# Optimization experiments

Measured on AMD Instinct MI355X. Metric: run time of the kernel, lower is better.

## Reference

```python
import jax, jax.numpy as jnp
import numpy as np

B = 4096      # number of graphs (segments)
D = 256       # node feature dim
N = B * 64    # total nodes across the batch


def setup_inputs() -> dict:
    key = jax.random.key(0)
    x = jax.random.normal(key, (N, D), dtype=jnp.float32)
    # ragged per-graph node counts: strictly positive, sum exactly to N
    rng = np.random.default_rng(0)
    sizes = 1 + rng.multinomial(N - B, np.full(B, 1.0 / B))
    feature_size_list = jnp.asarray(sizes, dtype=jnp.int64)
    return {"x": x, "feature_size_list": feature_size_list}


def reference(x, feature_size_list):
    # Fused segment-mean: one pass over x instead of a Python loop with cat.
    num_segments = feature_size_list.shape[0]  # static
    seg_ids = jnp.repeat(
        jnp.arange(num_segments), feature_size_list, total_repeat_length=x.shape[0]
    )
    sums = jax.ops.segment_sum(x, seg_ids, num_segments=num_segments)  # [B, D]
    return sums / feature_size_list[:, None].astype(x.dtype)
```

## Files before the change

kernel.cpp:

```cpp
#include <hip/hip_runtime.h>


#define NSEG 4096

__global__ __launch_bounds__(256) void scan_offsets_kernel(
    const int* __restrict__ sizes, int* __restrict__ offsets) {
    const int CHUNK = NSEG / 256;
    int tid = threadIdx.x;
    int base = tid * CHUNK;

    int local[CHUNK];
    int sum = 0;
#pragma unroll
    for (int i = 0; i < CHUNK; ++i) local[i] = sizes[base + i];
#pragma unroll
    for (int i = 0; i < CHUNK; ++i) {
        int v = local[i];
        local[i] = sum;
        sum += v;
    }

    __shared__ int sh[256];
    sh[tid] = sum;
    __syncthreads();
    for (int off = 1; off < 256; off <<= 1) {
        int v = (tid >= off) ? sh[tid - off] : 0;
        __syncthreads();
        sh[tid] += v;
        __syncthreads();
    }
    int excl = (tid == 0) ? 0 : sh[tid - 1];
#pragma unroll
    for (int i = 0; i < CHUNK; ++i) offsets[base + i] = excl + local[i];
}

__global__ __launch_bounds__(256) void seg_mean_kernel(
    const float* __restrict__ x,
    const int* __restrict__ sizes,
    const int* __restrict__ offsets,
    float* __restrict__ out) {
    int b = blockIdx.x;
    int size = sizes[b];
    size_t start = (size_t)offsets[b];

    int tx = threadIdx.x & 63;
    int ty = threadIdx.x >> 6;

    const float4* xr = reinterpret_cast<const float4*>(x) + start * 64 + tx;

    float4 a0 = make_float4(0.f, 0.f, 0.f, 0.f);
    float4 a1 = make_float4(0.f, 0.f, 0.f, 0.f);

    int r = ty;
    for (; r + 8 <= size; r += 8) {
        float4 v0 = xr[(size_t)r * 64];
        float4 v1 = xr[(size_t)(r + 4) * 64];
        a0.x += v0.x; a0.y += v0.y; a0.z += v0.z; a0.w += v0.w;
        a1.x += v1.x; a1.y += v1.y; a1.z += v1.z; a1.w += v1.w;
    }
    for (; r < size; r += 4) {
        float4 v0 = xr[(size_t)r * 64];
        a0.x += v0.x; a0.y += v0.y; a0.z += v0.z; a0.w += v0.w;
    }
    a0.x += a1.x; a0.y += a1.y; a0.z += a1.z; a0.w += a1.w;

    __shared__ float4 sh[256];
    sh[threadIdx.x] = a0;
    __syncthreads();

    if (ty == 0) {
        float4 b0 = sh[tx];
        float4 b1 = sh[tx + 64];
        float4 b2 = sh[tx + 128];
        float4 b3 = sh[tx + 192];
        float fs = (float)size;
        float4 o;
        o.x = (b0.x + b1.x + b2.x + b3.x) / fs;
        o.y = (b0.y + b1.y + b2.y + b3.y) / fs;
        o.z = (b0.z + b1.z + b2.z + b3.z) / fs;
        o.w = (b0.w + b1.w + b2.w + b3.w) / fs;
        reinterpret_cast<float4*>(out)[(size_t)b * 64 + tx] = o;
    }
}

extern "C" void kernel_launch(void* const* d_in, const int* in_sizes, int n_in,
                              void* d_out, int out_size, void* d_ws, size_t ws_size,
                              hipStream_t stream) {
    const float* x = (const float*)d_in[0];
    const int* sizes = (const int*)d_in[1];
    float* out = (float*)d_out;
    int* offsets = (int*)d_ws;

    scan_offsets_kernel<<<1, 256, 0, stream>>>(sizes, offsets);
    seg_mean_kernel<<<NSEG, 256, 0, stream>>>(x, sizes, offsets, out);
}
```

Measured before the change: 50.90 us.

## Fuse offset scan into segment-mean kernel and deepen load unrolling

Removes the separate single-block scan kernel. Each block now computes its own start offset by summing all preceding segment sizes with a wave-shuffle reduction, which saves a launch and a serial dependency. The cost is redundant work that grows with the block index, up to about 4096 int reads for the last block. The row loop is also unrolled to four independent accumulators, and loads and stores use nontemporal hints.

```diff
diff --git a/kernel.cpp b/kernel.cpp
--- a/kernel.cpp
+++ b/kernel.cpp
@@ -3,83 +3,68 @@
 
 #define NSEG 4096
 
-__global__ __launch_bounds__(256) void scan_offsets_kernel(
-    const int* __restrict__ sizes, int* __restrict__ offsets) {
-    const int CHUNK = NSEG / 256;
-    int tid = threadIdx.x;
-    int base = tid * CHUNK;
+typedef float f32x4 __attribute__((ext_vector_type(4)));
 
-    int local[CHUNK];
-    int sum = 0;
-#pragma unroll
-    for (int i = 0; i < CHUNK; ++i) local[i] = sizes[base + i];
-#pragma unroll
-    for (int i = 0; i < CHUNK; ++i) {
-        int v = local[i];
-        local[i] = sum;
-        sum += v;
-    }
-
-    __shared__ int sh[256];
-    sh[tid] = sum;
-    __syncthreads();
-    for (int off = 1; off < 256; off <<= 1) {
-        int v = (tid >= off) ? sh[tid - off] : 0;
-        __syncthreads();
-        sh[tid] += v;
-        __syncthreads();
-    }
-    int excl = (tid == 0) ? 0 : sh[tid - 1];
-#pragma unroll
-    for (int i = 0; i < CHUNK; ++i) offsets[base + i] = excl + local[i];
-}
-
-__global__ __launch_bounds__(256) void seg_mean_kernel(
+__global__ __launch_bounds__(256) void seg_mean_fused_kernel(
     const float* __restrict__ x,
     const int* __restrict__ sizes,
-    const int* __restrict__ offsets,
     float* __restrict__ out) {
-    int b = blockIdx.x;
-    int size = sizes[b];
-    size_t start = (size_t)offsets[b];
+    const int b   = blockIdx.x;
+    const int tid = threadIdx.x;
+    const int tx  = tid & 63;
+    const int ty  = tid >> 6;
 
-    int tx = threadIdx.x & 63;
-    int ty = threadIdx.x >> 6;
+    int partial = 0;
+    for (int i = tid; i < b; i += 256) partial += sizes[i];
+#pragma unroll
+    for (int off = 32; off > 0; off >>= 1)
+        partial += __shfl_down(partial, off, 64);
 
-    const float4* xr = reinterpret_cast<const float4*>(x) + start * 64 + tx;
+    __shared__ int swave[4];
+    __shared__ int s_start;
+    if (tx == 0) swave[ty] = partial;
+    __syncthreads();
+    if (tid == 0) s_start = swave[0] + swave[1] + swave[2] + swave[3];
+    __syncthreads();
 
-    float4 a0 = make_float4(0.f, 0.f, 0.f, 0.f);
-    float4 a1 = make_float4(0.f, 0.f, 0.f, 0.f);
+    const int size     = sizes[b];
+    const size_t start = (size_t)s_start;
+
+    const f32x4* xr = reinterpret_cast<const f32x4*>(x) + start * 64 + tx;
+
+    f32x4 a0 = {0.f, 0.f, 0.f, 0.f};
+    f32x4 a1 = {0.f, 0.f, 0.f, 0.f};
+    f32x4 a2 = {0.f, 0.f, 0.f, 0.f};
+    f32x4 a3 = {0.f, 0.f, 0.f, 0.f};
 
     int r = ty;
-    for (; r + 8 <= size; r += 8) {
-        float4 v0 = xr[(size_t)r * 64];
-        float4 v1 = xr[(size_t)(r + 4) * 64];
-        a0.x += v0.x; a0.y += v0.y; a0.z += v0.z; a0.w += v0.w;
-        a1.x += v1.x; a1.y += v1.y; a1.z += v1.z; a1.w += v1.w;
+    for (; r + 16 <= size; r += 16) {
+        f32x4 v0 = __builtin_nontemporal_load(&xr[(size_t)r * 64]);
+        f32x4 v1 = __builtin_nontemporal_load(&xr[(size_t)(r + 4) * 64]);
+        f32x4 v2 = __builtin_nontemporal_load(&xr[(size_t)(r + 8) * 64]);
+        f32x4 v3 = __builtin_nontemporal_load(&xr[(size_t)(r + 12) * 64]);
+        a0 += v0;
+        a1 += v1;
+        a2 += v2;
+        a3 += v3;
     }
     for (; r < size; r += 4) {
-        float4 v0 = xr[(size_t)r * 64];
-        a0.x += v0.x; a0.y += v0.y; a0.z += v0.z; a0.w += v0.w;
+        f32x4 v0 = __builtin_nontemporal_load(&xr[(size_t)r * 64]);
+        a0 += v0;
     }
-    a0.x += a1.x; a0.y += a1.y; a0.z += a1.z; a0.w += a1.w;
+    a0 += a1;
+    a2 += a3;
+    a0 += a2;
 
-    __shared__ float4 sh[256];
-    sh[threadIdx.x] = a0;
+    __shared__ f32x4 sh[256];
+    sh[tid] = a0;
     __syncthreads();
 
     if (ty == 0) {
-        float4 b0 = sh[tx];
-        float4 b1 = sh[tx + 64];
-        float4 b2 = sh[tx + 128];
-        float4 b3 = sh[tx + 192];
+        f32x4 s = sh[tx] + sh[tx + 64] + sh[tx + 128] + sh[tx + 192];
         float fs = (float)size;
-        float4 o;
-        o.x = (b0.x + b1.x + b2.x + b3.x) / fs;
-        o.y = (b0.y + b1.y + b2.y + b3.y) / fs;
-        o.z = (b0.z + b1.z + b2.z + b3.z) / fs;
-        o.w = (b0.w + b1.w + b2.w + b3.w) / fs;
-        reinterpret_cast<float4*>(out)[(size_t)b * 64 + tx] = o;
+        f32x4 o = s / fs;
+        __builtin_nontemporal_store(o, &reinterpret_cast<f32x4*>(out)[(size_t)b * 64 + tx]);
     }
 }
 
@@ -89,8 +74,6 @@
     const float* x = (const float*)d_in[0];
     const int* sizes = (const int*)d_in[1];
     float* out = (float*)d_out;
-    int* offsets = (int*)d_ws;
 
-    scan_offsets_kernel<<<1, 256, 0, stream>>>(sizes, offsets);
-    seg_mean_kernel<<<NSEG, 256, 0, stream>>>(x, sizes, offsets, out);
+    seg_mean_fused_kernel<<<NSEG, 256, 0, stream>>>(x, sizes, out);
 }
```

Result: faster. 48.41 us (-4.9%).
